# Kernel tuning notes

Hardware: AMD Instinct MI355X
Metric: run time of the kernel (lower is better)

The kernel has to match this reference:

```python
import jax, jax.numpy as jnp
import numpy as np

VOCAB = 10000
EMBED = 100
SEQ = 80
BATCH = 256
UNITS = 2048


def setup_inputs() -> dict:
    key = jax.random.key(0)
    ks = jax.random.split(key, 10)
    s = lambda fan_in: 1.0 / np.sqrt(fan_in)
    inputs = jax.random.randint(ks[0], (BATCH, SEQ), 0, VOCAB, dtype=jnp.int32)
    emb = jax.random.normal(ks[1], (VOCAB, EMBED), dtype=jnp.float32) * 0.05
    W0 = jax.random.normal(ks[2], (EMBED, UNITS), dtype=jnp.float32) * s(EMBED)
    U0 = jax.random.normal(ks[3], (UNITS, UNITS), dtype=jnp.float32) * s(UNITS)
    b0 = jnp.zeros((UNITS,), dtype=jnp.float32)
    W1 = jax.random.normal(ks[4], (UNITS, UNITS), dtype=jnp.float32) * s(UNITS)
    U1 = jax.random.normal(ks[5], (UNITS, UNITS), dtype=jnp.float32) * s(UNITS)
    b1 = jnp.zeros((UNITS,), dtype=jnp.float32)
    Wo = jax.random.normal(ks[6], (UNITS, 1), dtype=jnp.float32) * s(UNITS)
    bo = jnp.zeros((1,), dtype=jnp.float32)
    return {"inputs": inputs, "emb": emb, "W0": W0, "U0": U0, "b0": b0,
            "W1": W1, "U1": U1, "b1": b1, "Wo": Wo, "bo": bo}


def reference(inputs, emb, W0, U0, b0, W1, U1, b1, Wo, bo):
    # Embedding lookup: [B, T, E]
    x = emb[inputs]
    # time-major for scan: [T, B, E]
    xt = jnp.transpose(x, (1, 0, 2))
    B = inputs.shape[0]
    h0_init = jnp.zeros((B, U0.shape[0]), dtype=x.dtype)
    h1_init = jnp.zeros((B, U1.shape[0]), dtype=x.dtype)

    def step(carry, x_t):
        h0, h1 = carry
        # SimpleRNNCell: h' = tanh(x W + h U + b); dropout inactive (training=None)
        h0 = jnp.tanh(x_t @ W0 + h0 @ U0 + b0)
        h1 = jnp.tanh(h0 @ W1 + h1 @ U1 + b1)
        return (h0, h1), None

    (_, h1_final), _ = jax.lax.scan(step, (h0_init, h1_init), xt)
    logits = h1_final @ Wo + bo  # [B, 1]
    return jax.nn.sigmoid(logits)
```

## Files before the change

kernel.cpp:

```cpp
#include <hip/hip_runtime.h>


typedef _Float16 f16;
typedef _Float16 f16x2 __attribute__((ext_vector_type(2)));
typedef _Float16 f16x8 __attribute__((ext_vector_type(8)));
typedef float    f32x4 __attribute__((ext_vector_type(4)));

#define NWG    256
#define SEQ    80
#define EPAD   128
#define NKC0   68
#define NKC1   128

#define FLAGS_OFF  0
#define HBUF_OFF   1024
#define HBUF_ONE   (256 * 4096 * 2)
#define B0S_OFF    (HBUF_OFF + 2 * HBUF_ONE)
#define B0S_SIZE   (2048 * NKC0 * 32 * 2)
#define B1S_OFF    (B0S_OFF + B0S_SIZE)
#define B1S_SIZE   (2048 * NKC1 * 32 * 2)
#define XP_OFF     (B1S_OFF + B1S_SIZE)
#define XP_SIZE    (SEQ * 256 * EPAD * 2)
#define WS_NEED    ((size_t)XP_OFF + XP_SIZE)

__device__ __forceinline__ float tanh_fast(float x) {
  x = fminf(15.f, fmaxf(-15.f, x));
  float e = __expf(2.f * x);
  return (e - 1.f) * __builtin_amdgcn_rcpf(e + 1.f);
}

__device__ __forceinline__ f16x8 ldg16_coh(const f16* p) {
  f16x8 r;
  asm volatile("global_load_dwordx4 %0, %1, off sc0 sc1" : "=v"(r) : "v"(p));
  return r;
}
__device__ __forceinline__ f16x8 ldg16(const f16* p) {
  f16x8 r;
  asm volatile("global_load_dwordx4 %0, %1, off" : "=v"(r) : "v"(p));
  return r;
}
__device__ __forceinline__ void stg16_coh(f16* p, f16x8 v) {
  asm volatile("global_store_dwordx4 %0, %1, off sc0 sc1" :: "v"(p), "v"(v) : "memory");
}
#define VWAIT(name, n)                                                        \
__device__ __forceinline__ void name(f16x8 (&a)[4], f16x8 (&b)[4]) {          \
  asm volatile("s_waitcnt vmcnt(" #n ")"                                      \
    : "+v"(a[0]), "+v"(a[1]), "+v"(a[2]), "+v"(a[3]),                         \
      "+v"(b[0]), "+v"(b[1]), "+v"(b[2]), "+v"(b[3]) :: "memory");            \
}
VWAIT(vwait16, 16)
VWAIT(vwait8, 8)
VWAIT(vwait0, 0)

__device__ __forceinline__ void gbar(int* flags, int target) {
  asm volatile("s_waitcnt vmcnt(0)" ::: "memory");
  __syncthreads();
  if (threadIdx.x == 0)
    __hip_atomic_store(&flags[blockIdx.x], target, __ATOMIC_RELAXED,
                       __HIP_MEMORY_SCOPE_AGENT);
  if (threadIdx.x < NWG) {
    while (__hip_atomic_load(&flags[threadIdx.x], __ATOMIC_RELAXED,
                             __HIP_MEMORY_SCOPE_AGENT) < target)
      __builtin_amdgcn_s_sleep(2);
  }
  __syncthreads();
}

__global__ __launch_bounds__(256) void fmt_weights(
    const float* __restrict__ W0, const float* __restrict__ U0,
    const float* __restrict__ W1, const float* __restrict__ U1,
    char* __restrict__ ws)
{
  int frag = blockIdx.x * 4 + (threadIdx.x >> 6);
  int lane = threadIdx.x & 63, lr = lane & 15, lk = (lane >> 4) * 8;
  f16x8 h;
  f16* dst;
  if (frag < 32 * NKC0 * 4) {
    int slice = frag / (NKC0 * 4), rem = frag % (NKC0 * 4);
    int kcg = rem >> 2, n16 = rem & 3;
    int col = slice * 64 + n16 * 16 + lr;
#pragma unroll
    for (int j = 0; j < 8; ++j) {
      int k = kcg * 32 + lk + j;
      float v;
      if (k < 2048) v = U0[(size_t)k * 2048 + col];
      else { int e = k - 2048; v = (e < 100) ? W0[(size_t)e * 2048 + col] : 0.f; }
      h[j] = (f16)v;
    }
    dst = (f16*)(ws + B0S_OFF) + (size_t)frag * 512;
  } else {
    int fr = frag - 32 * NKC0 * 4;
    int slice = fr / (NKC1 * 4), rem = fr % (NKC1 * 4);
    int kcg = rem >> 2, n16 = rem & 3;
    int col = slice * 64 + n16 * 16 + lr;
#pragma unroll
    for (int j = 0; j < 8; ++j) {
      int k = kcg * 32 + lk + j;
      float v = (k < 2048) ? W1[(size_t)k * 2048 + col]
                           : U1[(size_t)(k - 2048) * 2048 + col];
      h[j] = (f16)v;
    }
    dst = (f16*)(ws + B1S_OFF) + (size_t)fr * 512;
  }
  *(f16x8*)(dst + lane * 8) = h;
}

__global__ __launch_bounds__(256) void embed_k(
    const int* __restrict__ inputs, const float* __restrict__ emb,
    char* __restrict__ ws)
{
  int r = blockIdx.x * 4 + (threadIdx.x >> 6);
  int lane = threadIdx.x & 63;
  int t = r >> 8, b = r & 255;
  int idx = inputs[b * SEQ + t];
  int e = lane * 2;
  f16x2 h;
  if (e < 100) {
    const float* src = emb + (size_t)idx * 100 + e;
    h[0] = (f16)src[0]; h[1] = (f16)src[1];
  } else { h[0] = (f16)0.f; h[1] = (f16)0.f; }
  *(f16x2*)(ws + XP_OFF + ((size_t)r * EPAD + e) * 2) = h;
}

template <int NKC, bool L0T>
__device__ __forceinline__ void ktile(
    const f16* __restrict__ Hr, const f16* __restrict__ Xp,
    const f16* __restrict__ bp, const size_t* aoff, const size_t* xoff,
    int kb, f32x4 (&acc)[4][4])
{
  f16x8 A[3][4], B[3][4];
  auto LD = [&](int kc, f16x8 (&a)[4], f16x8 (&b)[4]) {
#pragma unroll
    for (int cf = 0; cf < 4; ++cf)
      b[cf] = ldg16(bp + (size_t)kc * 2048 + cf * 512);
    int kk = kb + kc * 32;
    if (L0T && kk >= 2048) {
#pragma unroll
      for (int rf = 0; rf < 4; ++rf)
        a[rf] = ldg16_coh(Xp + xoff[rf] + (kk - 2048));
    } else {
#pragma unroll
      for (int rf = 0; rf < 4; ++rf)
        a[rf] = ldg16_coh(Hr + aoff[rf] + kk);
    }
  };
  auto ST = [&](f16x8 (&a)[4], f16x8 (&b)[4]) {
#pragma unroll
    for (int cf = 0; cf < 4; ++cf)
#pragma unroll
      for (int rf = 0; rf < 4; ++rf)
        acc[rf][cf] = __builtin_amdgcn_mfma_f32_16x16x32_f16(
            a[rf], b[cf], acc[rf][cf], 0, 0, 0);
  };

  LD(0, A[0], B[0]);
  if (NKC > 1) LD(1, A[1], B[1]);
#pragma unroll
  for (int kc = 0; kc < NKC; ++kc) {
    f16x8 (&a)[4] = A[kc % 3];
    f16x8 (&b)[4] = B[kc % 3];
    if (kc + 2 < NKC) { LD(kc + 2, A[(kc + 2) % 3], B[(kc + 2) % 3]); vwait16(a, b); }
    else if (kc + 1 < NKC) vwait8(a, b);
    else vwait0(a, b);
    ST(a, b);
  }
}

__global__ __launch_bounds__(512, 2) void rnn_persist(
    const float* __restrict__ b0v, const float* __restrict__ b1v,
    char* __restrict__ ws)
{
  __shared__ f32x4 red[8][8][64];
  __shared__ f16 T[64 * 64];

  const int bid = blockIdx.x;
  const int tid = threadIdx.x;
  const int wv = tid >> 6, lane = tid & 63;
  const int lr = lane & 15, lk = (lane >> 4) * 8;

  int* flags = (int*)(ws + FLAGS_OFF);
  f16* HbA = (f16*)(ws + HBUF_OFF);
  f16* HbB = (f16*)(ws + HBUF_OFF + HBUF_ONE);
  const f16* Xp = (const f16*)(ws + XP_OFF);

  const bool isL0 = bid < 128;
  const int u = isL0 ? bid : bid - 128;
  const int cslice = (u & 7) * 4 + ((u >> 3) & 3);
  const int m0 = (u >> 5) * 64;
  const int n0 = cslice * 64;
  const f16* Bst = (const f16*)(ws + (isL0 ? B0S_OFF : B1S_OFF));
  const int NKCg = isL0 ? NKC0 : NKC1;
  const int kcgb = isL0 ? wv * 9 : wv * 16;
  const int kb   = kcgb * 32;
  const float* bias = isL0 ? b0v : b1v;
  const int outh = isL0 ? 0 : 2048;

  const f16* bp = Bst + ((size_t)cslice * NKCg + kcgb) * 2048 + lane * 8;

  size_t aoff[4], xoff[4];
#pragma unroll
  for (int rf = 0; rf < 4; ++rf)
    aoff[rf] = (size_t)(m0 + rf * 16 + lr) * 4096 + lk;

  for (int p = 0; p <= 80; ++p) {
    const f16* Hr = ((p + 1) & 1) ? HbB : HbA;
    f16*       Hw = (p & 1) ? HbB : HbA;
    const bool active = isL0 ? (p < 80) : true;
    const bool fzero  = (!isL0) && (p == 0);

    f32x4 acc[4][4];
#pragma unroll
    for (int a = 0; a < 4; ++a)
#pragma unroll
      for (int b = 0; b < 4; ++b) acc[a][b] = {0.f, 0.f, 0.f, 0.f};

    if (active && !fzero) {
      if (isL0) {
#pragma unroll
        for (int rf = 0; rf < 4; ++rf)
          xoff[rf] = ((size_t)p * 256 + m0 + rf * 16 + lr) * EPAD + lk;
        if (wv < 7) ktile<9, true>(Hr, Xp, bp, aoff, xoff, kb, acc);
        else        ktile<5, true>(Hr, Xp, bp, aoff, xoff, kb, acc);
      } else {
        ktile<16, false>(Hr, Xp, bp, aoff, xoff, kb, acc);
      }
    }

    if (active) {
#pragma unroll
      for (int t = 0; t < 2; ++t) {
        if (t) __syncthreads();
#pragma unroll
        for (int rr = 0; rr < 2; ++rr)
#pragma unroll
          for (int cf = 0; cf < 4; ++cf)
            red[wv][rr * 4 + cf][lane] = acc[2 * t + rr][cf];
        __syncthreads();
        {
          const int rf = 2 * t + (wv >> 2), cf = wv & 3;
          f32x4 s = red[0][wv][lane];
#pragma unroll
          for (int ow = 1; ow < 8; ++ow) s += red[ow][wv][lane];
          const int tcol = cf * 16 + lr;
          const float bv = bias[n0 + tcol];
          const int trow = rf * 16 + (lane >> 4) * 4;
#pragma unroll
          for (int r = 0; r < 4; ++r) {
            const float v = fzero ? 0.f : tanh_fast(s[r] + bv);
            T[(trow + r) * 64 + (tcol ^ (((trow + r) & 3) << 4))] = (f16)v;
          }
        }
      }
      __syncthreads();
      {
        const int row = tid >> 3, c8 = (tid & 7) * 8;
        f16x8 val = *(const f16x8*)(T + row * 64 + (c8 ^ ((row & 3) << 4)));
        stg16_coh(Hw + (size_t)(m0 + row) * 4096 + outh + n0 + c8, val);
      }
    }
    if (p < 80) gbar(flags, p + 1);
  }
}

__global__ __launch_bounds__(256) void logits_k(
    const char* __restrict__ ws, const float* __restrict__ Wo,
    const float* __restrict__ bo, float* __restrict__ out)
{
  int row = blockIdx.x * 4 + (threadIdx.x >> 6);
  int lane = threadIdx.x & 63;
  const f16* h1 = (const f16*)(ws + HBUF_OFF) + (size_t)row * 4096 + 2048;
  float s = 0.f;
#pragma unroll
  for (int it = 0; it < 4; ++it) {
    int k = it * 512 + lane * 8;
    f16x8 hv = *(const f16x8*)(h1 + k);
    const float4* wp = (const float4*)(Wo + k);
    float4 w0 = wp[0], w1 = wp[1];
    s += (float)hv[0] * w0.x + (float)hv[1] * w0.y + (float)hv[2] * w0.z + (float)hv[3] * w0.w;
    s += (float)hv[4] * w1.x + (float)hv[5] * w1.y + (float)hv[6] * w1.z + (float)hv[7] * w1.w;
  }
#pragma unroll
  for (int off = 32; off > 0; off >>= 1) s += __shfl_down(s, off);
  if (lane == 0) out[row] = 1.f / (1.f + __expf(-(s + bo[0])));
}

extern "C" void kernel_launch(void* const* d_in, const int* in_sizes, int n_in,
                              void* d_out, int out_size, void* d_ws, size_t ws_size,
                              hipStream_t stream)
{
  (void)in_sizes; (void)n_in; (void)out_size;
  const int*   inputs = (const int*)d_in[0];
  const float* emb    = (const float*)d_in[1];
  const float* W0     = (const float*)d_in[2];
  const float* U0     = (const float*)d_in[3];
  const float* b0     = (const float*)d_in[4];
  const float* W1     = (const float*)d_in[5];
  const float* U1     = (const float*)d_in[6];
  const float* b1     = (const float*)d_in[7];
  const float* Wo     = (const float*)d_in[8];
  const float* bo     = (const float*)d_in[9];
  char* ws = (char*)d_ws;
  if (ws_size < WS_NEED) return;

  hipMemsetAsync(ws, 0, HBUF_OFF + 2 * HBUF_ONE, stream);
  fmt_weights<<<6272, 256, 0, stream>>>(W0, U0, W1, U1, ws);
  embed_k<<<5120, 256, 0, stream>>>(inputs, emb, ws);
  rnn_persist<<<NWG, 512, 0, stream>>>(b0, b1, ws);
  logits_k<<<64, 256, 0, stream>>>(ws, Wo, bo, (float*)d_out);
}
```

Before: 3.216 ms.

## Use per-timestep hidden-state slots so recurrent loads can skip coherent cache bypass

```diff
diff --git a/kernel.cpp b/kernel.cpp
--- a/kernel.cpp
+++ b/kernel.cpp
@@ -12,16 +12,18 @@
 #define NKC0   68
 #define NKC1   128
 
-#define FLAGS_OFF  0
-#define HBUF_OFF   1024
-#define HBUF_ONE   (256 * 4096 * 2)
-#define B0S_OFF    (HBUF_OFF + 2 * HBUF_ONE)
-#define B0S_SIZE   (2048 * NKC0 * 32 * 2)
-#define B1S_OFF    (B0S_OFF + B0S_SIZE)
-#define B1S_SIZE   (2048 * NKC1 * 32 * 2)
-#define XP_OFF     (B1S_OFF + B1S_SIZE)
-#define XP_SIZE    (SEQ * 256 * EPAD * 2)
-#define WS_NEED    ((size_t)XP_OFF + XP_SIZE)
+#define FLAGS_OFF   0
+#define B0S_OFF     1024
+#define B0S_SIZE    (2176 * 2048 * 2)
+#define B1S_OFF     (B0S_OFF + B0S_SIZE)
+#define B1S_SIZE    (4096 * 2048 * 2)
+#define XP_OFF      (B1S_OFF + B1S_SIZE)
+#define XP_SIZE     (SEQ * 256 * EPAD * 2)
+#define H0_OFF      (XP_OFF + XP_SIZE)
+#define HSLOT       (256 * 2048 * 2)
+#define HSLOT_H     (256 * 2048)
+#define WS_FULL     ((size_t)H0_OFF + (size_t)162 * HSLOT)
+#define WS_MIN      ((size_t)H0_OFF + (size_t)6 * HSLOT)
 
 __device__ __forceinline__ float tanh_fast(float x) {
   x = fminf(15.f, fmaxf(-15.f, x));
@@ -122,9 +124,9 @@
   *(f16x2*)(ws + XP_OFF + ((size_t)r * EPAD + e) * 2) = h;
 }
 
-template <int NKC, bool L0T>
+template <int NKC, bool L0T, bool COH>
 __device__ __forceinline__ void ktile(
-    const f16* __restrict__ Hr, const f16* __restrict__ Xp,
+    const f16* __restrict__ Ab, const f16* __restrict__ Xp,
     const f16* __restrict__ bp, const size_t* aoff, const size_t* xoff,
     int kb, f32x4 (&acc)[4][4])
 {
@@ -137,11 +139,13 @@
     if (L0T && kk >= 2048) {
 #pragma unroll
       for (int rf = 0; rf < 4; ++rf)
-        a[rf] = ldg16_coh(Xp + xoff[rf] + (kk - 2048));
+        a[rf] = ldg16(Xp + xoff[rf] + (kk - 2048));
     } else {
 #pragma unroll
-      for (int rf = 0; rf < 4; ++rf)
-        a[rf] = ldg16_coh(Hr + aoff[rf] + kk);
+      for (int rf = 0; rf < 4; ++rf) {
+        const f16* p = Ab + aoff[rf] + kk;
+        if (COH) a[rf] = ldg16_coh(p); else a[rf] = ldg16(p);
+      }
     }
   };
   auto ST = [&](f16x8 (&a)[4], f16x8 (&b)[4]) {
@@ -166,6 +170,7 @@
   }
 }
 
+template <int NBUF, bool COH>
 __global__ __launch_bounds__(512, 2) void rnn_persist(
     const float* __restrict__ b0v, const float* __restrict__ b1v,
     char* __restrict__ ws)
@@ -179,8 +184,8 @@
   const int lr = lane & 15, lk = (lane >> 4) * 8;
 
   int* flags = (int*)(ws + FLAGS_OFF);
-  f16* HbA = (f16*)(ws + HBUF_OFF);
-  f16* HbB = (f16*)(ws + HBUF_OFF + HBUF_ONE);
+  f16* H0b = (f16*)(ws + H0_OFF);
+  f16* H1b = H0b + (size_t)NBUF * HSLOT_H;
   const f16* Xp = (const f16*)(ws + XP_OFF);
 
   const bool isL0 = bid < 128;
@@ -189,22 +194,21 @@
   const int m0 = (u >> 5) * 64;
   const int n0 = cslice * 64;
   const f16* Bst = (const f16*)(ws + (isL0 ? B0S_OFF : B1S_OFF));
-  const int NKCg = isL0 ? NKC0 : NKC1;
   const int kcgb = isL0 ? wv * 9 : wv * 16;
-  const int kb   = kcgb * 32;
   const float* bias = isL0 ? b0v : b1v;
-  const int outh = isL0 ? 0 : 2048;
-
-  const f16* bp = Bst + ((size_t)cslice * NKCg + kcgb) * 2048 + lane * 8;
+
+  const f16* bp = Bst + ((size_t)cslice * (isL0 ? NKC0 : NKC1) + kcgb) * 2048 + lane * 8;
 
   size_t aoff[4], xoff[4];
 #pragma unroll
   for (int rf = 0; rf < 4; ++rf)
-    aoff[rf] = (size_t)(m0 + rf * 16 + lr) * 4096 + lk;
+    aoff[rf] = (size_t)(m0 + rf * 16 + lr) * 2048 + lk;
 
   for (int p = 0; p <= 80; ++p) {
-    const f16* Hr = ((p + 1) & 1) ? HbB : HbA;
-    f16*       Hw = (p & 1) ? HbB : HbA;
+    const f16* Hr0 = H0b + (size_t)(p % NBUF) * HSLOT_H;
+    const f16* Hr1 = H1b + (size_t)((p >= 1 ? (p - 1) % NBUF : 0)) * HSLOT_H;
+    f16* Hw = isL0 ? H0b + (size_t)((p + 1) % NBUF) * HSLOT_H
+                   : H1b + (size_t)(p % NBUF) * HSLOT_H;
     const bool active = isL0 ? (p < 80) : true;
     const bool fzero  = (!isL0) && (p == 0);
 
@@ -219,10 +223,11 @@
 #pragma unroll
         for (int rf = 0; rf < 4; ++rf)
           xoff[rf] = ((size_t)p * 256 + m0 + rf * 16 + lr) * EPAD + lk;
-        if (wv < 7) ktile<9, true>(Hr, Xp, bp, aoff, xoff, kb, acc);
-        else        ktile<5, true>(Hr, Xp, bp, aoff, xoff, kb, acc);
+        if (wv < 7) ktile<9, true, COH>(Hr0, Xp, bp, aoff, xoff, wv * 288, acc);
+        else        ktile<5, true, COH>(Hr0, Xp, bp, aoff, xoff, wv * 288, acc);
       } else {
-        ktile<16, false>(Hr, Xp, bp, aoff, xoff, kb, acc);
+        const f16* Ab = (wv < 4) ? Hr0 : Hr1;
+        ktile<16, false, COH>(Ab, Xp, bp, aoff, xoff, (wv & 3) * 512, acc);
       }
     }
 
@@ -255,7 +260,7 @@
       {
         const int row = tid >> 3, c8 = (tid & 7) * 8;
         f16x8 val = *(const f16x8*)(T + row * 64 + (c8 ^ ((row & 3) << 4)));
-        stg16_coh(Hw + (size_t)(m0 + row) * 4096 + outh + n0 + c8, val);
+        stg16_coh(Hw + (size_t)(m0 + row) * 2048 + n0 + c8, val);
       }
     }
     if (p < 80) gbar(flags, p + 1);
@@ -263,17 +268,17 @@
 }
 
 __global__ __launch_bounds__(256) void logits_k(
-    const char* __restrict__ ws, const float* __restrict__ Wo,
+    const f16* __restrict__ h1, const float* __restrict__ Wo,
     const float* __restrict__ bo, float* __restrict__ out)
 {
   int row = blockIdx.x * 4 + (threadIdx.x >> 6);
   int lane = threadIdx.x & 63;
-  const f16* h1 = (const f16*)(ws + HBUF_OFF) + (size_t)row * 4096 + 2048;
+  const f16* hr = h1 + (size_t)row * 2048;
   float s = 0.f;
 #pragma unroll
   for (int it = 0; it < 4; ++it) {
     int k = it * 512 + lane * 8;
-    f16x8 hv = *(const f16x8*)(h1 + k);
+    f16x8 hv = *(const f16x8*)(hr + k);
     const float4* wp = (const float4*)(Wo + k);
     float4 w0 = wp[0], w1 = wp[1];
     s += (float)hv[0] * w0.x + (float)hv[1] * w0.y + (float)hv[2] * w0.z + (float)hv[3] * w0.w;
@@ -300,11 +305,21 @@
   const float* Wo     = (const float*)d_in[8];
   const float* bo     = (const float*)d_in[9];
   char* ws = (char*)d_ws;
-  if (ws_size < WS_NEED) return;
-
-  hipMemsetAsync(ws, 0, HBUF_OFF + 2 * HBUF_ONE, stream);
+  if (ws_size < WS_MIN) return;
+
+  const bool full = (ws_size >= WS_FULL);
+  const int  nbuf = full ? 81 : 3;
+
+  hipMemsetAsync(ws + FLAGS_OFF, 0, 1024, stream);
+  hipMemsetAsync(ws + H0_OFF, 0, HSLOT, stream);
+  hipMemsetAsync(ws + H0_OFF + (size_t)nbuf * HSLOT, 0, HSLOT, stream);
+
   fmt_weights<<<6272, 256, 0, stream>>>(W0, U0, W1, U1, ws);
   embed_k<<<5120, 256, 0, stream>>>(inputs, emb, ws);
-  rnn_persist<<<NWG, 512, 0, stream>>>(b0, b1, ws);
-  logits_k<<<64, 256, 0, stream>>>(ws, Wo, bo, (float*)d_out);
-}
+  if (full) rnn_persist<81, false><<<NWG, 512, 0, stream>>>(b0, b1, ws);
+  else      rnn_persist<3,  true ><<<NWG, 512, 0, stream>>>(b0, b1, ws);
+
+  const f16* h1f = (const f16*)(ws + H0_OFF + (size_t)nbuf * HSLOT
+                                + (size_t)(80 % nbuf) * HSLOT);
+  logits_k<<<64, 256, 0, stream>>>(h1f, Wo, bo, (float*)d_out);
+}
```

Result: faster. 2.875 ms (-10.6%).
